# Kernel tuning notes

Measured on AMD Instinct MI355X. Metric: run time of the kernel, lower is better.

The kernel has to match this reference:

```python
import jax, jax.numpy as jnp
import numpy as np

N_ENT = 100000
N_REL = 12
D = 64
E = 1000000
LAYER_DIMS = [64, 32]


def _xavier(key, shape):
    fan_in, fan_out = shape[-1], shape[-2] if len(shape) >= 2 else shape[-1]
    std = np.sqrt(2.0 / (fan_in + fan_out)).astype(np.float32)
    return jax.random.normal(key, shape, jnp.float32) * std


def setup_inputs() -> dict:
    key = jax.random.key(0)
    ks = jax.random.split(key, 14)
    return {
        "entity_emb": _xavier(ks[0], (N_ENT, D)),
        "rel_emb": _xavier(ks[1], (N_REL, D)),
        "W_r": _xavier(ks[2], (N_REL, D, D)),
        "W1_0_w": _xavier(ks[3], (LAYER_DIMS[0], D)),
        "W1_0_b": jnp.zeros((LAYER_DIMS[0],), jnp.float32),
        "W2_0_w": _xavier(ks[4], (LAYER_DIMS[0], D)),
        "W2_0_b": jnp.zeros((LAYER_DIMS[0],), jnp.float32),
        "W1_1_w": _xavier(ks[5], (LAYER_DIMS[1], LAYER_DIMS[0])),
        "W1_1_b": jnp.zeros((LAYER_DIMS[1],), jnp.float32),
        "W2_1_w": _xavier(ks[6], (LAYER_DIMS[1], LAYER_DIMS[0])),
        "W2_1_b": jnp.zeros((LAYER_DIMS[1],), jnp.float32),
        "src": jax.random.randint(ks[7], (E,), 0, N_ENT, jnp.int32),
        "dst": jax.random.randint(ks[8], (E,), 0, N_ENT, jnp.int32),
        "etype": jax.random.randint(ks[9], (E,), 0, N_REL, jnp.int32),
    }


def reference(entity_emb, rel_emb, W_r, W1_0_w, W1_0_b, W2_0_w, W2_0_b,
              W1_1_w, W1_1_b, W2_1_w, W2_1_b, src, dst, etype):
    n = entity_emb.shape[0]

    # --- compute_attention: per-edge TransR scores, edge_softmax over dst ---
    # Instead of gathering W_r[etype] per edge ([E,D,D] is huge), project every
    # node by every relation matrix once: [N, R, Dr].
    proj = jnp.einsum('nd,kdr->nkr', entity_emb, W_r)
    tail = proj[src, etype]          # [E, Dr] (src projected by its edge's W_r)
    head = proj[dst, etype]          # [E, Dr]
    rel = rel_emb[etype]             # [E, Dr]
    logits = jnp.sum(tail * jnp.tanh(head + rel), axis=-1)  # [E]

    # edge softmax grouped by destination node (stable)
    m = jax.ops.segment_max(logits, dst, num_segments=n)
    ex = jnp.exp(logits - m[dst])
    den = jax.ops.segment_sum(ex, dst, num_segments=n)
    att = ex / den[dst]              # [E]

    # --- KGATLayer: gather-scale-scatter + bi-interaction (dropout = 0) ---
    def layer(x, W1w, W1b, W2w, W2b):
        h_n = jax.ops.segment_sum(x[src] * att[:, None], dst, num_segments=n)
        add = jax.nn.leaky_relu((x + h_n) @ W1w.T + W1b)
        mul = jax.nn.leaky_relu((x * h_n) @ W2w.T + W2b)
        return add + mul

    x0 = entity_emb
    x1 = layer(x0, W1_0_w, W1_0_b, W2_0_w, W2_0_b)
    x2 = layer(x1, W1_1_w, W1_1_b, W2_1_w, W2_1_b)
    # embedder concatenates the input and every layer output
    return jnp.concatenate([x0, x1, x2], axis=1)  # [N, 64+64+32]
```

## Files before the change

kernel.cpp:

```cpp
#include <hip/hip_runtime.h>
#include <hip/hip_bf16.h>
#include <math.h>


typedef __attribute__((ext_vector_type(8))) short short8;
typedef __attribute__((ext_vector_type(4))) float float4v;

__device__ __forceinline__ short f2bf(float f) {
  __hip_bfloat16 h = __float2bfloat16(f);
  return *(short*)&h;
}
__device__ __forceinline__ float bf2f(short s) {
  return __uint_as_float(((unsigned)(unsigned short)s) << 16);
}

#define LOG2E 1.4426950408889634f
#define BS1_TILE 2048

__global__ void k_prep(const float* __restrict__ emb, short* __restrict__ emb_h,
                       float* __restrict__ out,
                       const float* __restrict__ Wr, short* __restrict__ Bt,
                       const float* __restrict__ W10, const float* __restrict__ W20,
                       const float* __restrict__ W11, const float* __restrict__ W21,
                       short* __restrict__ w1h0, short* __restrict__ w1l0,
                       short* __restrict__ w2h0, short* __restrict__ w2l0,
                       short* __restrict__ w1h1, short* __restrict__ w1l1,
                       short* __restrict__ w2h1, short* __restrict__ w2l1,
                       const int* __restrict__ src, const int* __restrict__ dst,
                       const int* __restrict__ et, int* __restrict__ bcur,
                       uint2* __restrict__ stg, int nE, int bsh, int cap,
                       int nb1, int nb_cvt, int n4) {
  __shared__ int hist[256];
  __shared__ int base[256];
  int b = blockIdx.x, t = threadIdx.x;
  if (b < nb1) {
    hist[t] = 0;
    __syncthreads();
    int tile = b * BS1_TILE;
#pragma unroll
    for (int j = 0; j < BS1_TILE / 256; j++) {
      int e = tile + j * 256 + t;
      if (e < nE) atomicAdd(&hist[dst[e] >> bsh], 1);
    }
    __syncthreads();
    int cnt = hist[t];
    if (cnt > 0) base[t] = atomicAdd(&bcur[t], cnt);
    hist[t] = 0;
    __syncthreads();
#pragma unroll
    for (int j = 0; j < BS1_TILE / 256; j++) {
      int e = tile + j * 256 + t;
      if (e < nE) {
        int d = dst[e], bk = d >> bsh;
        int r = atomicAdd(&hist[bk], 1);
        stg[(size_t)bk * cap + base[bk] + r] =
            make_uint2((unsigned)src[e], (unsigned)d | ((unsigned)et[e] << 20));
      }
    }
    return;
  }
  int b2 = b - nb1;
  if (b2 < nb_cvt) {
    int i = b2 * 256 + t;
    if (i < n4) {
      float4 v = ((const float4*)emb)[i];
      union { short s[4]; uint2 u; } o;
      o.s[0] = f2bf(v.x); o.s[1] = f2bf(v.y); o.s[2] = f2bf(v.z); o.s[3] = f2bf(v.w);
      ((uint2*)emb_h)[i] = o.u;
      int node = i >> 4, ch = i & 15;
      *(float4*)(out + (size_t)node * 160 + ch * 4) = v;
    }
  } else if (b2 < nb_cvt + 12) {
    int k = b2 - nb_cvt;
    for (int i = t; i < 4096; i += 256) {
      int d = i >> 6, r = i & 63;
      Bt[k * 4096 + r * 64 + d] = f2bf(Wr[k * 4096 + i]);
    }
  } else {
    int i = (b2 - nb_cvt - 12) * 256 + t;
    const float* W; short* H; short* L; int j;
    if (i < 4096) { W = W10; H = w1h0; L = w1l0; j = i; }
    else if (i < 8192) { W = W20; H = w2h0; L = w2l0; j = i - 4096; }
    else if (i < 10240) { W = W11; H = w1h1; L = w1l1; j = i - 8192; }
    else if (i < 12288) { W = W21; H = w2h1; L = w2l1; j = i - 10240; }
    else return;
    float w = W[j];
    short hi = f2bf(w);
    H[j] = hi;
    L[j] = f2bf(w - bf2f(hi));
  }
}

__global__ __launch_bounds__(256) void k_projm(const short* __restrict__ A,
                                               const short* __restrict__ Bt,
                                               short* __restrict__ proj,
                                               int n_ent) {
  __shared__ unsigned short sh[4][32 * 72];
  int wave = threadIdx.x >> 6, lane = threadIdx.x & 63;
  int quad = lane >> 4, l16 = lane & 15;
  int m0 = blockIdx.x * 128 + wave * 32;
  unsigned short* W = &sh[wave][0];
  short8 a[2][2];
#pragma unroll
  for (int mt = 0; mt < 2; mt++)
#pragma unroll
    for (int kc = 0; kc < 2; kc++) {
      int row = m0 + mt * 16 + l16;
      int rr = row < n_ent ? row : 0;
      a[mt][kc] = *(const short8*)(A + (size_t)rr * 64 + kc * 32 + quad * 8);
    }
  for (int k = 0; k < 12; k++) {
    const short* B = Bt + k * 4096;
    short8 b[4][2];
#pragma unroll
    for (int nt = 0; nt < 4; nt++)
#pragma unroll
      for (int kc = 0; kc < 2; kc++)
        b[nt][kc] = *(const short8*)(B + (nt * 16 + l16) * 64 + kc * 32 + quad * 8);
    float4v acc[2][4];
#pragma unroll
    for (int mt = 0; mt < 2; mt++)
#pragma unroll
      for (int nt = 0; nt < 4; nt++)
        acc[mt][nt] = (float4v){0.f, 0.f, 0.f, 0.f};
#pragma unroll
    for (int kc = 0; kc < 2; kc++)
#pragma unroll
      for (int mt = 0; mt < 2; mt++)
#pragma unroll
        for (int nt = 0; nt < 4; nt++)
          acc[mt][nt] = __builtin_amdgcn_mfma_f32_16x16x32_bf16(
              a[mt][kc], b[nt][kc], acc[mt][nt], 0, 0, 0);
#pragma unroll
    for (int mt = 0; mt < 2; mt++)
#pragma unroll
      for (int nt = 0; nt < 4; nt++)
#pragma unroll
        for (int r = 0; r < 4; r++) {
          int row = mt * 16 + quad * 4 + r;
          int col = nt * 16 + l16;
          W[row * 72 + col] = (unsigned short)f2bf(acc[mt][nt][r]);
        }
    const size_t plane = (size_t)k * n_ent;
#pragma unroll
    for (int i = 0; i < 4; i++) {
      int row = (lane >> 3) + 8 * i;
      int cs = (lane & 7) * 8;
      short8 v = *(const short8*)(W + row * 72 + cs);
      int node = m0 + row;
      if (node < n_ent)
        *(short8*)(proj + (plane + node) * 64 + cs) = v;
    }
  }
}

__global__ __launch_bounds__(256) void k_bsort2(const uint2* __restrict__ stg,
                                                const int* __restrict__ bcur,
                                                int* __restrict__ row_ptr,
                                                uint2* __restrict__ csr2,
                                                int n, int bsh, int cap,
                                                int nbuck, int nE) {
  __shared__ int cnt[1024];
  __shared__ int sc[1024];
  __shared__ int bs[256];
  int b = blockIdx.x, t = threadIdx.x;
  int v = (t < nbuck) ? bcur[t] : 0;
  bs[t] = v;
  __syncthreads();
  for (int o = 1; o < 256; o <<= 1) {
    int a = (t >= o) ? bs[t - o] : 0;
    __syncthreads();
    bs[t] += a;
    __syncthreads();
  }
  int gbase = bs[b] - bcur[b];
  int lo = b << bsh;
  if (lo > n) lo = n;
  int hi = (b + 1) << bsh;
  if (hi > n) hi = n;
  int w = hi - lo;
#pragma unroll
  for (int j = 0; j < 4; j++) cnt[t + j * 256] = 0;
  __syncthreads();
  int m = bcur[b];
  const uint2* S = stg + (size_t)b * cap;
  for (int p = t; p < m; p += 256)
    atomicAdd(&cnt[(int)(S[p].y & 0xFFFFFu) - lo], 1);
  __syncthreads();
#pragma unroll
  for (int j = 0; j < 4; j++) sc[t + j * 256] = cnt[t + j * 256];
  __syncthreads();
  for (int o = 1; o < 1024; o <<= 1) {
    int a[4];
#pragma unroll
    for (int j = 0; j < 4; j++) {
      int i = t + j * 256;
      a[j] = (i >= o) ? sc[i - o] : 0;
    }
    __syncthreads();
#pragma unroll
    for (int j = 0; j < 4; j++) sc[t + j * 256] += a[j];
    __syncthreads();
  }
#pragma unroll
  for (int j = 0; j < 4; j++) {
    int i = t + j * 256;
    if (i < w) {
      int c0 = gbase + sc[i] - cnt[i];
      row_ptr[lo + i] = c0;
      cnt[i] = c0;
    }
  }
  if (b == nbuck - 1 && t == 0) row_ptr[n] = nE;
  __syncthreads();
  for (int p = t; p < m; p += 256) {
    uint2 vv = S[p];
    int d = (int)(vv.y & 0xFFFFFu);
    int pos = atomicAdd(&cnt[d - lo], 1);
    csr2[pos] = vv;
  }
}

__global__ __launch_bounds__(256) void k_logits(const short* __restrict__ ps,
                                                const float* __restrict__ rel_emb,
                                                uint2* csr2, int nE, int n_ent) {
  int t = threadIdx.x;
  int lane = t & 63;
  int sub = lane >> 3;
  int c8 = (lane & 7) * 8;
  int e0 = (blockIdx.x * 4 + (t >> 6)) * 32;
  if (e0 >= nE) return;
  int ku[4];
  short8 tl[4], hd[4];
#pragma unroll
  for (int u = 0; u < 4; u++) {
    int e = e0 + u * 8 + sub;
    int ee = e < nE ? e : nE - 1;
    uint2 c = csr2[ee];
    int s = (int)c.x;
    int d = (int)(c.y & 0xFFFFFu);
    int k = (int)(c.y >> 20);
    ku[u] = k;
    const size_t plane = (size_t)k * n_ent;
    tl[u] = *(const short8*)(ps + (plane + s) * 64 + c8);
    hd[u] = *(const short8*)(ps + (plane + d) * 64 + c8);
  }
  float v[4];
#pragma unroll
  for (int u = 0; u < 4; u++) {
    const float* rp = rel_emb + ku[u] * 64 + c8;
    float4 r0 = *(const float4*)rp;
    float4 r1 = *(const float4*)(rp + 4);
    float rr[8] = {r0.x, r0.y, r0.z, r0.w, r1.x, r1.y, r1.z, r1.w};
    float vv = 0.f;
#pragma unroll
    for (int q = 0; q < 8; q++) {
      float x = bf2f(hd[u][q]) + rr[q];
      float tt = __builtin_amdgcn_exp2f(x * (2.f * LOG2E));
      float r = __builtin_amdgcn_rcpf(tt + 1.f);
      float th = fmaf(-2.f, r, 1.f);
      vv = fmaf(bf2f(tl[u][q]), th, vv);
    }
    vv += __shfl_xor(vv, 1);
    vv += __shfl_xor(vv, 2);
    vv += __shfl_xor(vv, 4);
    v[u] = __builtin_amdgcn_exp2f(vv * LOG2E);
  }
  int uu = lane & 7;
  if (uu < 4) {
    float myv = v[0];
    if (uu == 1) myv = v[1];
    if (uu == 2) myv = v[2];
    if (uu == 3) myv = v[3];
    int e = e0 + uu * 8 + sub;
    if (e < nE) csr2[e].y = __float_as_uint(myv);
  }
}

__global__ __launch_bounds__(256) void k_agg(const short* __restrict__ xh,
                                             const int* __restrict__ row_ptr,
                                             const uint2* __restrict__ csr,
                                             float* __restrict__ hn, int n_ent) {
  int wave = threadIdx.x >> 6, lane = threadIdx.x & 63;
  int n = blockIdx.x * 4 + wave;
  if (n >= n_ent) return;
  int jb = row_ptr[n], je = row_ptr[n + 1];
  int deg = je - jb;
  if (deg == 0) {
    hn[(size_t)n * 64 + lane] = 0.f;
    return;
  }
  uint2 c = (lane < deg) ? csr[jb + lane] : make_uint2(0u, 0u);
  int sidx = (int)c.x;
  float exv = (lane < deg) ? __uint_as_float(c.y) : 0.f;
  float den = exv;
#pragma unroll
  for (int o = 32; o; o >>= 1) den += __shfl_xor(den, o);
  int m = deg < 64 ? deg : 64;
  float acc = 0.f;
  for (int j = 0; j < m; j += 8) {
    int s0 = __shfl(sidx, j), s1 = __shfl(sidx, j + 1);
    int s2 = __shfl(sidx, j + 2), s3 = __shfl(sidx, j + 3);
    int s4 = __shfl(sidx, j + 4), s5 = __shfl(sidx, j + 5);
    int s6 = __shfl(sidx, j + 6), s7 = __shfl(sidx, j + 7);
    float e0 = __shfl(exv, j), e1 = __shfl(exv, j + 1);
    float e2 = __shfl(exv, j + 2), e3 = __shfl(exv, j + 3);
    float e4 = __shfl(exv, j + 4), e5 = __shfl(exv, j + 5);
    float e6 = __shfl(exv, j + 6), e7 = __shfl(exv, j + 7);
    short g0 = xh[(size_t)s0 * 64 + lane];
    short g1 = xh[(size_t)s1 * 64 + lane];
    short g2 = xh[(size_t)s2 * 64 + lane];
    short g3 = xh[(size_t)s3 * 64 + lane];
    short g4 = xh[(size_t)s4 * 64 + lane];
    short g5 = xh[(size_t)s5 * 64 + lane];
    short g6 = xh[(size_t)s6 * 64 + lane];
    short g7 = xh[(size_t)s7 * 64 + lane];
    acc = fmaf(e0, bf2f(g0), acc); acc = fmaf(e1, bf2f(g1), acc);
    acc = fmaf(e2, bf2f(g2), acc); acc = fmaf(e3, bf2f(g3), acc);
    acc = fmaf(e4, bf2f(g4), acc); acc = fmaf(e5, bf2f(g5), acc);
    acc = fmaf(e6, bf2f(g6), acc); acc = fmaf(e7, bf2f(g7), acc);
  }
  if (deg > 64) {
    for (int jj = jb + 64; jj < je; jj++) {
      uint2 cc = csr[jj];
      float ee = __uint_as_float(cc.y);
      den += ee;
      acc = fmaf(ee, bf2f(xh[(size_t)cc.x * 64 + lane]), acc);
    }
  }
  hn[(size_t)n * 64 + lane] = acc / den;
}

template <int OD, bool FIRST>
__global__ __launch_bounds__(256) void k_upmfma(const float* __restrict__ x,
                                                const float* __restrict__ hn,
                                                const short* __restrict__ g1h,
                                                const short* __restrict__ g1l,
                                                const short* __restrict__ g2h,
                                                const short* __restrict__ g2l,
                                                const float* __restrict__ b1,
                                                const float* __restrict__ b2,
                                                float* __restrict__ out,
                                                float* __restrict__ x_next,
                                                short* __restrict__ xh_next,
                                                int n_ent) {
  constexpr int NT = OD / 16;
  constexpr int S = (OD == 64) ? 66 : 34;
  __shared__ short wbuf[4 * OD * 72];
  short* w1h = wbuf;
  short* w1l = wbuf + OD * 72;
  short* w2h = wbuf + 2 * OD * 72;
  short* w2l = wbuf + 3 * OD * 72;
  int t = threadIdx.x;
  for (int i = t; i < OD * 16; i += 256) {
    int o = i >> 4, dq = (i & 15) * 4;
    *(uint2*)(w1h + o * 72 + dq) = *(const uint2*)(g1h + o * 64 + dq);
    *(uint2*)(w1l + o * 72 + dq) = *(const uint2*)(g1l + o * 64 + dq);
    *(uint2*)(w2h + o * 72 + dq) = *(const uint2*)(g2h + o * 64 + dq);
    *(uint2*)(w2l + o * 72 + dq) = *(const uint2*)(g2l + o * 64 + dq);
  }
  int wave = t >> 6, lane = t & 63;
  int quad = lane >> 4, l16 = lane & 15;
  int m0 = blockIdx.x * 128 + wave * 32;
  float4v accA[2][NT], accM[2][NT];
#pragma unroll
  for (int mt = 0; mt < 2; mt++)
#pragma unroll
    for (int nt = 0; nt < NT; nt++) {
      accA[mt][nt] = (float4v){0.f, 0.f, 0.f, 0.f};
      accM[mt][nt] = (float4v){0.f, 0.f, 0.f, 0.f};
    }
  __syncthreads();
#pragma unroll
  for (int kc = 0; kc < 2; kc++) {
    short8 ah_add[2], al_add[2], ah_mul[2], al_mul[2];
#pragma unroll
    for (int mt = 0; mt < 2; mt++) {
      int row = m0 + mt * 16 + l16;
      int rr = row < n_ent ? row : 0;
      const float* xp = x + (size_t)rr * 64 + kc * 32 + quad * 8;
      const float* hp = hn + (size_t)rr * 64 + kc * 32 + quad * 8;
      float4 xa = *(const float4*)xp;
      float4 xb = *(const float4*)(xp + 4);
      float4 ha = *(const float4*)hp;
      float4 hb = *(const float4*)(hp + 4);
      float xs[8] = {xa.x, xa.y, xa.z, xa.w, xb.x, xb.y, xb.z, xb.w};
      float hs[8] = {ha.x, ha.y, ha.z, ha.w, hb.x, hb.y, hb.z, hb.w};
#pragma unroll
      for (int q = 0; q < 8; q++) {
        float s = xs[q] + hs[q];
        short shi = f2bf(s);
        ah_add[mt][q] = shi;
        al_add[mt][q] = f2bf(s - bf2f(shi));
        float p = xs[q] * hs[q];
        short phi = f2bf(p);
        ah_mul[mt][q] = phi;
        al_mul[mt][q] = f2bf(p - bf2f(phi));
      }
    }
#pragma unroll
    for (int nt = 0; nt < NT; nt++) {
      int boff = (nt * 16 + l16) * 72 + kc * 32 + quad * 8;
      short8 b1h = *(const short8*)(w1h + boff);
      short8 b1l = *(const short8*)(w1l + boff);
      short8 b2h = *(const short8*)(w2h + boff);
      short8 b2l = *(const short8*)(w2l + boff);
#pragma unroll
      for (int mt = 0; mt < 2; mt++) {
        accA[mt][nt] = __builtin_amdgcn_mfma_f32_16x16x32_bf16(
            ah_add[mt], b1h, accA[mt][nt], 0, 0, 0);
        accA[mt][nt] = __builtin_amdgcn_mfma_f32_16x16x32_bf16(
            al_add[mt], b1h, accA[mt][nt], 0, 0, 0);
        accA[mt][nt] = __builtin_amdgcn_mfma_f32_16x16x32_bf16(
            ah_add[mt], b1l, accA[mt][nt], 0, 0, 0);
        accM[mt][nt] = __builtin_amdgcn_mfma_f32_16x16x32_bf16(
            ah_mul[mt], b2h, accM[mt][nt], 0, 0, 0);
        accM[mt][nt] = __builtin_amdgcn_mfma_f32_16x16x32_bf16(
            al_mul[mt], b2h, accM[mt][nt], 0, 0, 0);
        accM[mt][nt] = __builtin_amdgcn_mfma_f32_16x16x32_bf16(
            ah_mul[mt], b2l, accM[mt][nt], 0, 0, 0);
      }
    }
  }
  __syncthreads();
  float* yt = (float*)wbuf + wave * 32 * S;
#pragma unroll
  for (int nt = 0; nt < NT; nt++) {
    int col = nt * 16 + l16;
    float bb1 = b1[col], bb2 = b2[col];
#pragma unroll
    for (int mt = 0; mt < 2; mt++) {
#pragma unroll
      for (int r = 0; r < 4; r++) {
        float aa = accA[mt][nt][r] + bb1;
        float mm = accM[mt][nt][r] + bb2;
        aa = aa > 0.f ? aa : 0.01f * aa;
        mm = mm > 0.f ? mm : 0.01f * mm;
        yt[(mt * 16 + quad * 4 + r) * S + col] = aa + mm;
      }
    }
  }
  constexpr int LPR = OD / 4;
  constexpr int RPI = 64 / LPR;
#pragma unroll
  for (int i = 0; i < 32 / RPI; i++) {
    int rloc = i * RPI + lane / LPR;
    int c4 = (lane % LPR) * 4;
    float4 v = *(const float4*)(yt + rloc * S + c4);
    int node = m0 + rloc;
    if (node < n_ent) {
      if constexpr (FIRST) {
        *(float4*)(out + (size_t)node * 160 + 64 + c4) = v;
        *(float4*)(x_next + (size_t)node * 64 + c4) = v;
        unsigned p0 = (unsigned)(unsigned short)f2bf(v.x) |
                      ((unsigned)(unsigned short)f2bf(v.y) << 16);
        unsigned p1 = (unsigned)(unsigned short)f2bf(v.z) |
                      ((unsigned)(unsigned short)f2bf(v.w) << 16);
        *(uint2*)(xh_next + (size_t)node * 64 + c4) = make_uint2(p0, p1);
      } else {
        *(float4*)(out + (size_t)node * 160 + 128 + c4) = v;
      }
    }
  }
}

extern "C" void kernel_launch(void* const* d_in, const int* in_sizes, int n_in,
                              void* d_out, int out_size, void* d_ws, size_t ws_size,
                              hipStream_t stream) {
  const float* emb = (const float*)d_in[0];
  const float* rel = (const float*)d_in[1];
  const float* Wr = (const float*)d_in[2];
  const float* W10w = (const float*)d_in[3];
  const float* W10b = (const float*)d_in[4];
  const float* W20w = (const float*)d_in[5];
  const float* W20b = (const float*)d_in[6];
  const float* W11w = (const float*)d_in[7];
  const float* W11b = (const float*)d_in[8];
  const float* W21w = (const float*)d_in[9];
  const float* W21b = (const float*)d_in[10];
  const int* src = (const int*)d_in[11];
  const int* dst = (const int*)d_in[12];
  const int* et = (const int*)d_in[13];
  int N = in_sizes[0] / 64;
  int E = in_sizes[11];
  float* out = (float*)d_out;

  int bsh = 9;
  while (((N + (1 << bsh) - 1) >> bsh) > 256) bsh++;
  int nbuck = (N + (1 << bsh) - 1) >> bsh;
  int cap = ((E / nbuck) * 3 / 2 + 1024 + 255) / 256 * 256;

  char* p = (char*)d_ws;
  auto alloc = [&](size_t bytes) -> char* {
    char* r = p;
    p += (bytes + 255) / 256 * 256;
    return r;
  };
  short* proj = (short*)alloc((size_t)N * 768 * 2);
  uint2* csr2 = (uint2*)alloc((size_t)E * 8);
  uint2* stg = (uint2*)alloc((size_t)nbuck * cap * 8);
  int* row_ptr = (int*)alloc((size_t)(N + 1) * 4);
  int* bcur = (int*)alloc(1024);
  float* hn = (float*)alloc((size_t)N * 64 * 4);
  float* x1 = (float*)alloc((size_t)N * 64 * 4);
  short* emb_h = (short*)alloc(((size_t)N + 128) * 64 * 2);
  short* x1h = (short*)alloc(((size_t)N + 128) * 64 * 2);
  short* Bt = (short*)alloc((size_t)12 * 4096 * 2);
  short* w1h0 = (short*)alloc(4096 * 2);
  short* w1l0 = (short*)alloc(4096 * 2);
  short* w2h0 = (short*)alloc(4096 * 2);
  short* w2l0 = (short*)alloc(4096 * 2);
  short* w1h1 = (short*)alloc(2048 * 2);
  short* w1l1 = (short*)alloc(2048 * 2);
  short* w2h1 = (short*)alloc(2048 * 2);
  short* w2l1 = (short*)alloc(2048 * 2);

  int n4 = N * 16;
  int nb_cvt = (n4 + 255) / 256;
  int nb1 = (E + BS1_TILE - 1) / BS1_TILE;

  hipMemsetAsync(bcur, 0, 1024, stream);
  k_prep<<<nb1 + nb_cvt + 60, 256, 0, stream>>>(
      emb, emb_h, out, Wr, Bt, W10w, W20w, W11w, W21w,
      w1h0, w1l0, w2h0, w2l0, w1h1, w1l1, w2h1, w2l1,
      src, dst, et, bcur, stg, E, bsh, cap, nb1, nb_cvt, n4);
  k_projm<<<(N + 127) / 128, 256, 0, stream>>>(emb_h, Bt, proj, N);
  k_bsort2<<<nbuck, 256, 0, stream>>>(stg, bcur, row_ptr, csr2, N, bsh, cap, nbuck, E);
  k_logits<<<(E + 127) / 128, 256, 0, stream>>>(proj, rel, csr2, E, N);
  k_agg<<<(N + 3) / 4, 256, 0, stream>>>(emb_h, row_ptr, csr2, hn, N);
  k_upmfma<64, true><<<(N + 127) / 128, 256, 0, stream>>>(
      emb, hn, w1h0, w1l0, w2h0, w2l0, W10b, W20b, out, x1, x1h, N);
  k_agg<<<(N + 3) / 4, 256, 0, stream>>>(x1h, row_ptr, csr2, hn, N);
  k_upmfma<32, false><<<(N + 127) / 128, 256, 0, stream>>>(
      x1, hn, w1h1, w1l1, w2h1, w2l1, W11b, W21b, out, nullptr, nullptr, N);
}
```

Baseline: 378.3 us.

## Merge projection GEMM and bucket sort into one launch with larger row tiles

Combines the per-relation projection GEMM and the CSR bucket-sort kernel into a single launch, with block index choosing which role a block plays, so the two independent stages can run side by side on the GPU and one launch boundary goes away. The projection blocks also grow from 32 to 64 rows per wave (256 rows per block), which raises accumulator register use and halves the number of GEMM blocks. Shared memory is a single buffer reused by both roles, so the sort blocks now get the larger allocation. Padding on the bf16 input buffers is increased to cover the larger tile's out-of-range reads.

```diff
diff --git a/kernel.cpp b/kernel.cpp
--- a/kernel.cpp
+++ b/kernel.cpp
@@ -91,18 +91,88 @@
   }
 }
 
-__global__ __launch_bounds__(256) void k_projm(const short* __restrict__ A,
-                                               const short* __restrict__ Bt,
-                                               short* __restrict__ proj,
-                                               int n_ent) {
-  __shared__ unsigned short sh[4][32 * 72];
-  int wave = threadIdx.x >> 6, lane = threadIdx.x & 63;
+__global__ __launch_bounds__(256) void k_projb2(const short* __restrict__ A,
+                                                const short* __restrict__ Bt,
+                                                short* __restrict__ proj,
+                                                int n_ent,
+                                                const uint2* __restrict__ stg,
+                                                const int* __restrict__ bcur,
+                                                int* __restrict__ row_ptr,
+                                                uint2* __restrict__ csr2,
+                                                int nbg, int bsh, int cap,
+                                                int nbuck, int nE) {
+  __shared__ char smem[4 * 64 * 72 * 2];
+  int bid = blockIdx.x, t = threadIdx.x;
+  if (bid >= nbg) {
+    int b = bid - nbg;
+    int* cnt = (int*)smem;
+    int* sc = cnt + 1024;
+    int* bs = sc + 1024;
+    int v = (t < nbuck) ? bcur[t] : 0;
+    bs[t] = v;
+    __syncthreads();
+    for (int o = 1; o < 256; o <<= 1) {
+      int a = (t >= o) ? bs[t - o] : 0;
+      __syncthreads();
+      bs[t] += a;
+      __syncthreads();
+    }
+    int gbase = bs[b] - bcur[b];
+    int n = n_ent;
+    int lo = b << bsh;
+    if (lo > n) lo = n;
+    int hi = (b + 1) << bsh;
+    if (hi > n) hi = n;
+    int w = hi - lo;
+#pragma unroll
+    for (int j = 0; j < 4; j++) cnt[t + j * 256] = 0;
+    __syncthreads();
+    int m = bcur[b];
+    const uint2* S = stg + (size_t)b * cap;
+    for (int p = t; p < m; p += 256)
+      atomicAdd(&cnt[(int)(S[p].y & 0xFFFFFu) - lo], 1);
+    __syncthreads();
+#pragma unroll
+    for (int j = 0; j < 4; j++) sc[t + j * 256] = cnt[t + j * 256];
+    __syncthreads();
+    for (int o = 1; o < 1024; o <<= 1) {
+      int a[4];
+#pragma unroll
+      for (int j = 0; j < 4; j++) {
+        int i = t + j * 256;
+        a[j] = (i >= o) ? sc[i - o] : 0;
+      }
+      __syncthreads();
+#pragma unroll
+      for (int j = 0; j < 4; j++) sc[t + j * 256] += a[j];
+      __syncthreads();
+    }
+#pragma unroll
+    for (int j = 0; j < 4; j++) {
+      int i = t + j * 256;
+      if (i < w) {
+        int c0 = gbase + sc[i] - cnt[i];
+        row_ptr[lo + i] = c0;
+        cnt[i] = c0;
+      }
+    }
+    if (b == nbuck - 1 && t == 0) row_ptr[n] = nE;
+    __syncthreads();
+    for (int p = t; p < m; p += 256) {
+      uint2 vv = S[p];
+      int d = (int)(vv.y & 0xFFFFFu);
+      int pos = atomicAdd(&cnt[d - lo], 1);
+      csr2[pos] = vv;
+    }
+    return;
+  }
+  int wave = t >> 6, lane = t & 63;
   int quad = lane >> 4, l16 = lane & 15;
-  int m0 = blockIdx.x * 128 + wave * 32;
-  unsigned short* W = &sh[wave][0];
-  short8 a[2][2];
-#pragma unroll
-  for (int mt = 0; mt < 2; mt++)
+  int m0 = bid * 256 + wave * 64;
+  unsigned short* W = (unsigned short*)smem + wave * 64 * 72;
+  short8 a[4][2];
+#pragma unroll
+  for (int mt = 0; mt < 4; mt++)
 #pragma unroll
     for (int kc = 0; kc < 2; kc++) {
       int row = m0 + mt * 16 + l16;
@@ -117,22 +187,22 @@
 #pragma unroll
       for (int kc = 0; kc < 2; kc++)
         b[nt][kc] = *(const short8*)(B + (nt * 16 + l16) * 64 + kc * 32 + quad * 8);
-    float4v acc[2][4];
-#pragma unroll
-    for (int mt = 0; mt < 2; mt++)
+    float4v acc[4][4];
+#pragma unroll
+    for (int mt = 0; mt < 4; mt++)
 #pragma unroll
       for (int nt = 0; nt < 4; nt++)
         acc[mt][nt] = (float4v){0.f, 0.f, 0.f, 0.f};
 #pragma unroll
     for (int kc = 0; kc < 2; kc++)
 #pragma unroll
-      for (int mt = 0; mt < 2; mt++)
+      for (int mt = 0; mt < 4; mt++)
 #pragma unroll
         for (int nt = 0; nt < 4; nt++)
           acc[mt][nt] = __builtin_amdgcn_mfma_f32_16x16x32_bf16(
               a[mt][kc], b[nt][kc], acc[mt][nt], 0, 0, 0);
 #pragma unroll
-    for (int mt = 0; mt < 2; mt++)
+    for (int mt = 0; mt < 4; mt++)
 #pragma unroll
       for (int nt = 0; nt < 4; nt++)
 #pragma unroll
@@ -143,7 +213,7 @@
         }
     const size_t plane = (size_t)k * n_ent;
 #pragma unroll
-    for (int i = 0; i < 4; i++) {
+    for (int i = 0; i < 8; i++) {
       int row = (lane >> 3) + 8 * i;
       int cs = (lane & 7) * 8;
       short8 v = *(const short8*)(W + row * 72 + cs);
@@ -151,73 +221,6 @@
       if (node < n_ent)
         *(short8*)(proj + (plane + node) * 64 + cs) = v;
     }
-  }
-}
-
-__global__ __launch_bounds__(256) void k_bsort2(const uint2* __restrict__ stg,
-                                                const int* __restrict__ bcur,
-                                                int* __restrict__ row_ptr,
-                                                uint2* __restrict__ csr2,
-                                                int n, int bsh, int cap,
-                                                int nbuck, int nE) {
-  __shared__ int cnt[1024];
-  __shared__ int sc[1024];
-  __shared__ int bs[256];
-  int b = blockIdx.x, t = threadIdx.x;
-  int v = (t < nbuck) ? bcur[t] : 0;
-  bs[t] = v;
-  __syncthreads();
-  for (int o = 1; o < 256; o <<= 1) {
-    int a = (t >= o) ? bs[t - o] : 0;
-    __syncthreads();
-    bs[t] += a;
-    __syncthreads();
-  }
-  int gbase = bs[b] - bcur[b];
-  int lo = b << bsh;
-  if (lo > n) lo = n;
-  int hi = (b + 1) << bsh;
-  if (hi > n) hi = n;
-  int w = hi - lo;
-#pragma unroll
-  for (int j = 0; j < 4; j++) cnt[t + j * 256] = 0;
-  __syncthreads();
-  int m = bcur[b];
-  const uint2* S = stg + (size_t)b * cap;
-  for (int p = t; p < m; p += 256)
-    atomicAdd(&cnt[(int)(S[p].y & 0xFFFFFu) - lo], 1);
-  __syncthreads();
-#pragma unroll
-  for (int j = 0; j < 4; j++) sc[t + j * 256] = cnt[t + j * 256];
-  __syncthreads();
-  for (int o = 1; o < 1024; o <<= 1) {
-    int a[4];
-#pragma unroll
-    for (int j = 0; j < 4; j++) {
-      int i = t + j * 256;
-      a[j] = (i >= o) ? sc[i - o] : 0;
-    }
-    __syncthreads();
-#pragma unroll
-    for (int j = 0; j < 4; j++) sc[t + j * 256] += a[j];
-    __syncthreads();
-  }
-#pragma unroll
-  for (int j = 0; j < 4; j++) {
-    int i = t + j * 256;
-    if (i < w) {
-      int c0 = gbase + sc[i] - cnt[i];
-      row_ptr[lo + i] = c0;
-      cnt[i] = c0;
-    }
-  }
-  if (b == nbuck - 1 && t == 0) row_ptr[n] = nE;
-  __syncthreads();
-  for (int p = t; p < m; p += 256) {
-    uint2 vv = S[p];
-    int d = (int)(vv.y & 0xFFFFFu);
-    int pos = atomicAdd(&cnt[d - lo], 1);
-    csr2[pos] = vv;
   }
 }
 
@@ -503,8 +506,8 @@
   int* bcur = (int*)alloc(1024);
   float* hn = (float*)alloc((size_t)N * 64 * 4);
   float* x1 = (float*)alloc((size_t)N * 64 * 4);
-  short* emb_h = (short*)alloc(((size_t)N + 128) * 64 * 2);
-  short* x1h = (short*)alloc(((size_t)N + 128) * 64 * 2);
+  short* emb_h = (short*)alloc(((size_t)N + 256) * 64 * 2);
+  short* x1h = (short*)alloc(((size_t)N + 256) * 64 * 2);
   short* Bt = (short*)alloc((size_t)12 * 4096 * 2);
   short* w1h0 = (short*)alloc(4096 * 2);
   short* w1l0 = (short*)alloc(4096 * 2);
@@ -518,14 +521,15 @@
   int n4 = N * 16;
   int nb_cvt = (n4 + 255) / 256;
   int nb1 = (E + BS1_TILE - 1) / BS1_TILE;
+  int nbg = (N + 255) / 256;
 
   hipMemsetAsync(bcur, 0, 1024, stream);
   k_prep<<<nb1 + nb_cvt + 60, 256, 0, stream>>>(
       emb, emb_h, out, Wr, Bt, W10w, W20w, W11w, W21w,
       w1h0, w1l0, w2h0, w2l0, w1h1, w1l1, w2h1, w2l1,
       src, dst, et, bcur, stg, E, bsh, cap, nb1, nb_cvt, n4);
-  k_projm<<<(N + 127) / 128, 256, 0, stream>>>(emb_h, Bt, proj, N);
-  k_bsort2<<<nbuck, 256, 0, stream>>>(stg, bcur, row_ptr, csr2, N, bsh, cap, nbuck, E);
+  k_projb2<<<nbg + nbuck, 256, 0, stream>>>(
+      emb_h, Bt, proj, N, stg, bcur, row_ptr, csr2, nbg, bsh, cap, nbuck, E);
   k_logits<<<(E + 127) / 128, 256, 0, stream>>>(proj, rel, csr2, E, N);
   k_agg<<<(N + 3) / 4, 256, 0, stream>>>(emb_h, row_ptr, csr2, hn, N);
   k_upmfma<64, true><<<(N + 127) / 128, 256, 0, stream>>>(
```

Measured after the change: 338.2 us. 10.6% less time.
